# Kernel optimization log

Hardware: AMD Instinct MI355X
Metric: run time of the kernel (lower is better)

The kernel has to match this reference:

```python
import jax, jax.numpy as jnp
from jax import lax
import numpy as np

NUM_ITERS = 100
LEARNING_RATE = 0.1


def setup_inputs() -> dict:
    key = jax.random.key(0)
    replicates = jax.random.normal(key, (64, 500000), dtype=jnp.float32)
    return {"replicates": replicates}


def reference(replicates):
    """Vectorized per-replicate SGD on scalar x minimizing mean((data - x)^2).

    Faithful to the original: x starts at 0, each iteration computes the full
    MSE-reduction gradient grad = mean(2*(x - data)) over the replicate's data,
    then applies a plain SGD step. All K replicates run in lockstep (they are
    independent in the original loop), and the num_iters loop is a lax.scan.
    """
    K = replicates.shape[0]
    x0 = jnp.zeros((K,), dtype=replicates.dtype)

    def step(x, _):
        # grad of mean((data - x)^2) w.r.t. scalar x, per replicate: (K,)
        grad = jnp.mean(2.0 * (x[:, None] - replicates), axis=1)
        return x - LEARNING_RATE * grad, None

    x_final, _ = lax.scan(step, x0, None, length=NUM_ITERS)
    return x_final
```

## Files before the change

kernel.cpp:

```cpp
#include <hip/hip_runtime.h>


#define ROWS 64
#define COLS 500000
#define VEC4 (COLS / 4)
#define BLOCKS_PER_ROW 32
#define THREADS 256

__global__ __launch_bounds__(THREADS)
void row_partial_sum(const float* __restrict__ in, double* __restrict__ partial) {
    const int row = blockIdx.y;
    const int seg = blockIdx.x;
    const float4* rp = reinterpret_cast<const float4*>(in + (size_t)row * COLS);

    double acc = 0.0;
    for (int i = seg * THREADS + threadIdx.x; i < VEC4; i += BLOCKS_PER_ROW * THREADS) {
        float4 v = rp[i];
        acc += (double)v.x + (double)v.y + (double)v.z + (double)v.w;
    }

    #pragma unroll
    for (int off = 32; off > 0; off >>= 1)
        acc += __shfl_down(acc, off, 64);

    __shared__ double wsum[THREADS / 64];
    const int lane = threadIdx.x & 63;
    const int wave = threadIdx.x >> 6;
    if (lane == 0) wsum[wave] = acc;
    __syncthreads();
    if (threadIdx.x == 0) {
        double s = 0.0;
        #pragma unroll
        for (int w = 0; w < THREADS / 64; ++w) s += wsum[w];
        partial[row * BLOCKS_PER_ROW + seg] = s;
    }
}

__global__ void finalize(const double* __restrict__ partial, float* __restrict__ out) {
    const int r = threadIdx.x;
    if (r < ROWS) {
        double s = 0.0;
        #pragma unroll
        for (int b = 0; b < BLOCKS_PER_ROW; ++b) s += partial[r * BLOCKS_PER_ROW + b];
        const double m = s / (double)COLS;
        double f = 1.0;
        #pragma unroll
        for (int t = 0; t < 100; ++t) f *= 0.8;
        out[r] = (float)(m * (1.0 - f));
    }
}

extern "C" void kernel_launch(void* const* d_in, const int* in_sizes, int n_in,
                              void* d_out, int out_size, void* d_ws, size_t ws_size,
                              hipStream_t stream) {
    const float* in = (const float*)d_in[0];
    float* out = (float*)d_out;
    double* partial = (double*)d_ws;

    dim3 grid(BLOCKS_PER_ROW, ROWS);
    hipLaunchKernelGGL(row_partial_sum, grid, dim3(THREADS), 0, stream, in, partial);
    hipLaunchKernelGGL(finalize, dim3(1), dim3(64), 0, stream, partial, out);
}
```

Before: 179.0 us.

## Fuse finalize into reduction via float atomics and unroll loads four-way

Removes the separate finalize kernel by having each block scale its partial sum by the closed-form SGD factor and atomically add it into the output, which is zeroed with a memset first. The streaming loop is also unrolled four ways with independent accumulators to keep more loads in flight. This trades a kernel launch for a memset plus float atomics, which makes the summation order nondeterministic and does the cross-block sum in float instead of double.

```diff
diff --git a/kernel.cpp b/kernel.cpp
--- a/kernel.cpp
+++ b/kernel.cpp
@@ -4,49 +4,46 @@
 #define ROWS 64
 #define COLS 500000
 #define VEC4 (COLS / 4)
-#define BLOCKS_PER_ROW 32
+#define SEGS 32
 #define THREADS 256
+#define STRIDE (SEGS * THREADS)
 
 __global__ __launch_bounds__(THREADS)
-void row_partial_sum(const float* __restrict__ in, double* __restrict__ partial) {
-    const int row = blockIdx.y;
-    const int seg = blockIdx.x;
-    const float4* rp = reinterpret_cast<const float4*>(in + (size_t)row * COLS);
+void row_mean_sgd(const float* __restrict__ in, float* __restrict__ out) {
+    const int row = blockIdx.x >> 5;
+    const int seg = blockIdx.x & (SEGS - 1);
+    const float4* __restrict__ rp =
+        reinterpret_cast<const float4*>(in + (size_t)row * COLS);
 
-    double acc = 0.0;
-    for (int i = seg * THREADS + threadIdx.x; i < VEC4; i += BLOCKS_PER_ROW * THREADS) {
+    double a0 = 0.0, a1 = 0.0, a2 = 0.0, a3 = 0.0;
+    int i = seg * THREADS + threadIdx.x;
+    for (; i + 3 * STRIDE < VEC4; i += 4 * STRIDE) {
+        float4 v0 = rp[i];
+        float4 v1 = rp[i + STRIDE];
+        float4 v2 = rp[i + 2 * STRIDE];
+        float4 v3 = rp[i + 3 * STRIDE];
+        a0 += (double)v0.x + (double)v0.y + (double)v0.z + (double)v0.w;
+        a1 += (double)v1.x + (double)v1.y + (double)v1.z + (double)v1.w;
+        a2 += (double)v2.x + (double)v2.y + (double)v2.z + (double)v2.w;
+        a3 += (double)v3.x + (double)v3.y + (double)v3.z + (double)v3.w;
+    }
+    for (; i < VEC4; i += STRIDE) {
         float4 v = rp[i];
-        acc += (double)v.x + (double)v.y + (double)v.z + (double)v.w;
+        a0 += (double)v.x + (double)v.y + (double)v.z + (double)v.w;
     }
+    double acc = (a0 + a1) + (a2 + a3);
 
     #pragma unroll
     for (int off = 32; off > 0; off >>= 1)
         acc += __shfl_down(acc, off, 64);
 
     __shared__ double wsum[THREADS / 64];
-    const int lane = threadIdx.x & 63;
-    const int wave = threadIdx.x >> 6;
-    if (lane == 0) wsum[wave] = acc;
+    if ((threadIdx.x & 63) == 0) wsum[threadIdx.x >> 6] = acc;
     __syncthreads();
     if (threadIdx.x == 0) {
-        double s = 0.0;
-        #pragma unroll
-        for (int w = 0; w < THREADS / 64; ++w) s += wsum[w];
-        partial[row * BLOCKS_PER_ROW + seg] = s;
-    }
-}
-
-__global__ void finalize(const double* __restrict__ partial, float* __restrict__ out) {
-    const int r = threadIdx.x;
-    if (r < ROWS) {
-        double s = 0.0;
-        #pragma unroll
-        for (int b = 0; b < BLOCKS_PER_ROW; ++b) s += partial[r * BLOCKS_PER_ROW + b];
-        const double m = s / (double)COLS;
-        double f = 1.0;
-        #pragma unroll
-        for (int t = 0; t < 100; ++t) f *= 0.8;
-        out[r] = (float)(m * (1.0 - f));
+        double s = (wsum[0] + wsum[1]) + (wsum[2] + wsum[3]);
+        const double FACTOR = (1.0 - 2.0370359763344314e-10) / (double)COLS;
+        atomicAdd(out + row, (float)(s * FACTOR));
     }
 }
 
@@ -55,9 +52,8 @@
                               hipStream_t stream) {
     const float* in = (const float*)d_in[0];
     float* out = (float*)d_out;
-    double* partial = (double*)d_ws;
 
-    dim3 grid(BLOCKS_PER_ROW, ROWS);
-    hipLaunchKernelGGL(row_partial_sum, grid, dim3(THREADS), 0, stream, in, partial);
-    hipLaunchKernelGGL(finalize, dim3(1), dim3(64), 0, stream, partial, out);
+    hipMemsetAsync(out, 0, (size_t)out_size * sizeof(float), stream);
+    hipLaunchKernelGGL(row_mean_sgd, dim3(ROWS * SEGS), dim3(THREADS), 0, stream,
+                       in, out);
 }
```

After: 182.5 us. Within noise of the previous version (+2.0%).
